# Optimization experiments

Hardware: AMD Instinct MI355X
Metric: run time of the kernel (lower is better)

Reference implementation:

```python
import jax, jax.numpy as jnp
import numpy as np
from jax import lax

T = 256        # sentence length
V = 50000      # vocab
NT = 50        # POS tags
NL = 40        # dependency labels
WD, TD = 300, 100
IN = WD + TD   # 400, LSTM input & hidden size
H = IN
BI = 2 * H     # 800, biLSTM output per token
MI = 2 * BI    # 1600, MLP input/hidden size


def setup_inputs() -> dict:
    key = jax.random.key(0)
    ks = jax.random.split(key, 32)
    s = 0.05
    d = {
        'words': jax.random.randint(ks[0], (T,), 0, V),
        'tags': jax.random.randint(ks[1], (T,), 0, NT),
        'arcs': jax.random.randint(ks[2], (T + 1,), 0, T + 1),
        'h0': jax.random.normal(ks[3], (4, 1, H), jnp.float32),
        'c0': jax.random.normal(ks[4], (4, 1, H), jnp.float32),
        'word_emb': jax.random.normal(ks[5], (V, WD), jnp.float32) * s,
        'tag_emb': jax.random.normal(ks[6], (NT, TD), jnp.float32) * s,
        # LSTM layer 0: input IN; layer 1: input BI. Leading dim 2 = directions (fwd, rev).
        'Wih0': jax.random.normal(ks[7], (2, 4 * H, IN), jnp.float32) * s,
        'Whh0': jax.random.normal(ks[8], (2, 4 * H, H), jnp.float32) * s,
        'bih0': jax.random.normal(ks[9], (2, 4 * H), jnp.float32) * s,
        'bhh0': jax.random.normal(ks[10], (2, 4 * H), jnp.float32) * s,
        'Wih1': jax.random.normal(ks[11], (2, 4 * H, BI), jnp.float32) * s,
        'Whh1': jax.random.normal(ks[12], (2, 4 * H, H), jnp.float32) * s,
        'bih1': jax.random.normal(ks[13], (2, 4 * H), jnp.float32) * s,
        'bhh1': jax.random.normal(ks[14], (2, 4 * H), jnp.float32) * s,
        # arc-score MLP: 1600 -> 1600 -> 1 (Linear, Tanh, Linear)
        'Wa1': jax.random.normal(ks[15], (MI, MI), jnp.float32) * s,
        'ba1': jax.random.normal(ks[16], (MI,), jnp.float32) * s,
        'Wa2': jax.random.normal(ks[17], (1, MI), jnp.float32) * s,
        'ba2': jax.random.normal(ks[18], (1,), jnp.float32) * s,
        # label MLP: 1600 -> 1600 -> 40
        'Wl1': jax.random.normal(ks[19], (MI, MI), jnp.float32) * s,
        'bl1': jax.random.normal(ks[20], (MI,), jnp.float32) * s,
        'Wl2': jax.random.normal(ks[21], (NL, MI), jnp.float32) * s,
        'bl2': jax.random.normal(ks[22], (NL,), jnp.float32) * s,
    }
    return d


def _lstm_dir(x, Wih, Whh, bih, bhh, h, c):
    # x: [T, in]; returns [T, H]. Torch gate order i, f, g, o.
    xg = x @ Wih.T + (bih + bhh)  # precompute input projection: [T, 4H]

    def step(carry, xt):
        h, c = carry
        g = xt + h @ Whh.T
        i, f, gg, o = jnp.split(g, 4, axis=-1)
        i, f, o = jax.nn.sigmoid(i), jax.nn.sigmoid(f), jax.nn.sigmoid(o)
        c = f * c + i * jnp.tanh(gg)
        h = o * jnp.tanh(c)
        return (h, c), h

    (_, _), ys = lax.scan(step, (h, c), xg)
    return ys


def _bilstm_layer(x, Wih, Whh, bih, bhh, h0f, c0f, h0b, c0b):
    fwd = _lstm_dir(x, Wih[0], Whh[0], bih[0], bhh[0], h0f, c0f)
    bwd = _lstm_dir(x[::-1], Wih[1], Whh[1], bih[1], bhh[1], h0b, c0b)[::-1]
    return jnp.concatenate([fwd, bwd], axis=-1)


def _mlp(z, W1, b1, W2, b2):
    return jnp.tanh(z @ W1.T + b1) @ W2.T + b2


def reference(words, tags, arcs, h0, c0, word_emb, tag_emb,
              Wih0, Whh0, bih0, bhh0, Wih1, Whh1, bih1, bhh1,
              Wa1, ba1, Wa2, ba2, Wl1, bl1, Wl2, bl2):
    n = words.shape[0]
    x = jnp.concatenate([word_emb[words], tag_emb[tags]], axis=-1)  # [T, 400]
    x1 = _bilstm_layer(x, Wih0, Whh0, bih0, bhh0, h0[0, 0], c0[0, 0], h0[1, 0], c0[1, 0])
    hV = _bilstm_layer(x1, Wih1, Whh1, bih1, bhh1, h0[2, 0], c0[2, 0], h0[3, 0], c0[3, 0])  # [T, 800]

    # All-pairs arc scores: feats[h, d] = concat(hV[h], hV[d]) -> MLP -> scalar.
    hh = jnp.broadcast_to(hV[:, None, :], (n, n, BI))
    dd = jnp.broadcast_to(hV[None, :, :], (n, n, BI))
    feats = jnp.concatenate([hh, dd], axis=-1)  # [T, T, 1600]
    raw = _mlp(feats, Wa1, ba1, Wa2, ba2)[..., 0]  # [T, T]
    raw = raw * (1.0 - jnp.eye(n, dtype=raw.dtype))  # head == dep left at 0
    scores = jnp.zeros((n + 1, n + 1), raw.dtype).at[1:, 1:].set(raw).at[0, 0].set(1.0)

    # Labels: for token i with gold head h (1-based), concat(hV[i], hV[h-1]); head==0 -> zeros.
    heads = arcs[1:]
    idx = jnp.clip(heads - 1, 0, n - 1)
    lf = jnp.concatenate([hV, hV[idx]], axis=-1)  # [T, 1600]
    lab = _mlp(lf, Wl1, bl1, Wl2, bl2)  # [T, 40]
    lab = jnp.where((heads == 0)[:, None], jnp.zeros_like(lab), lab)
    return (scores, lab)
```

## Files before the change

### kernel.cpp

```cpp
#include <hip/hip_runtime.h>

typedef unsigned int   u32;
typedef unsigned long long u64;

__device__ __forceinline__ float fast_tanh(float x) {
    x = fminf(fmaxf(x, -15.f), 15.f);
    float e = __expf(2.f * x);
    return __fdividef(e - 1.f, e + 1.f);
}

#define OF_XG   ((size_t)0)
#define OF_H    (OF_XG + 3276800)
#define OF_PQ   (OF_H  + 1638400)
#define OF_U    (OF_PQ + 3276800)

__device__ __forceinline__ float4 hist4(const u64* __restrict__ hist, int t, int k) {
    const u64* p = (k < 400) ? hist + (size_t)t * 400 + k
                             : hist + 102400 + (size_t)(255 - t) * 400 + (k - 400);
    ulonglong2 a = *(const ulonglong2*)p;
    ulonglong2 b = *(const ulonglong2*)(p + 2);
    return make_float4(__uint_as_float((u32)a.x), __uint_as_float((u32)a.y),
                       __uint_as_float((u32)b.x), __uint_as_float((u32)b.y));
}

__global__ __launch_bounds__(256)
void gemm_embed_kernel(const int* __restrict__ words, const int* __restrict__ tags,
                       const float* __restrict__ wemb, const float* __restrict__ temb,
                       const float* __restrict__ B,
                       const float* __restrict__ bias1, const float* __restrict__ bias2,
                       float* __restrict__ C) {
    int t0 = blockIdx.x * 64;
    int n0 = blockIdx.y * 64;
    int tid = threadIdx.x;
    int tx = tid & 15, ty = tid >> 4;
    int lr = tid >> 2, lk = (tid & 3) * 4;
    __shared__ float As[16][68];
    __shared__ float Bs[16][68];
    float acc[4][4] = {};

    int t = t0 + lr;
    const float* arow0 = wemb + (size_t)words[t] * 300;
    const float* arow1 = temb + (size_t)tags[t] * 100 - 300;

    for (int k0 = 0; k0 < 400; k0 += 16) {
        int k = k0 + lk;
        float4 av = (k < 300) ? *(const float4*)(arow0 + k) : *(const float4*)(arow1 + k);
        float4 bv = *(const float4*)(B + (size_t)(n0 + lr) * 400 + k);
        __syncthreads();
        As[lk + 0][lr] = av.x; As[lk + 1][lr] = av.y; As[lk + 2][lr] = av.z; As[lk + 3][lr] = av.w;
        Bs[lk + 0][lr] = bv.x; Bs[lk + 1][lr] = bv.y; Bs[lk + 2][lr] = bv.z; Bs[lk + 3][lr] = bv.w;
        __syncthreads();
        #pragma unroll
        for (int kk = 0; kk < 16; ++kk) {
            float4 a4 = *(const float4*)&As[kk][ty * 4];
            float4 b4 = *(const float4*)&Bs[kk][tx * 4];
            acc[0][0] += a4.x * b4.x; acc[0][1] += a4.x * b4.y; acc[0][2] += a4.x * b4.z; acc[0][3] += a4.x * b4.w;
            acc[1][0] += a4.y * b4.x; acc[1][1] += a4.y * b4.y; acc[1][2] += a4.y * b4.z; acc[1][3] += a4.y * b4.w;
            acc[2][0] += a4.z * b4.x; acc[2][1] += a4.z * b4.y; acc[2][2] += a4.z * b4.z; acc[2][3] += a4.z * b4.w;
            acc[3][0] += a4.w * b4.x; acc[3][1] += a4.w * b4.y; acc[3][2] += a4.w * b4.z; acc[3][3] += a4.w * b4.w;
        }
    }
    float bs[4];
    #pragma unroll
    for (int j = 0; j < 4; ++j) {
        int n = n0 + tx * 4 + j;
        bs[j] = bias1[n] + bias2[n];
    }
    #pragma unroll
    for (int i = 0; i < 4; ++i) {
        int tr = t0 + ty * 4 + i;
        float4 o;
        o.x = acc[i][0] + bs[0]; o.y = acc[i][1] + bs[1];
        o.z = acc[i][2] + bs[2]; o.w = acc[i][3] + bs[3];
        *(float4*)(C + (size_t)tr * 3200 + n0 + tx * 4) = o;
    }
}

__global__ __launch_bounds__(256)
void gemm_hist_kernel(const u64* __restrict__ hist, const int* __restrict__ arcs,
                      const float* __restrict__ B, int ldb, int boff,
                      const float* __restrict__ bias1, const float* __restrict__ bias2,
                      float* __restrict__ C, int ldc, int K, int act) {
    int t0 = blockIdx.x * 64;
    int n0 = blockIdx.y * 64;
    int tid = threadIdx.x;
    int tx = tid & 15, ty = tid >> 4;
    int lr = tid >> 2, lk = (tid & 3) * 4;
    __shared__ float As[16][68];
    __shared__ float Bs[16][68];
    float acc[4][4] = {};

    int t = t0 + lr;
    int tind = t;
    if (arcs) {
        int h = arcs[1 + t];
        tind = min(max(h - 1, 0), 255);
    }

    for (int k0 = 0; k0 < K; k0 += 16) {
        int k = k0 + lk;
        int tt = (k < 800) ? t : tind;
        int kk2 = (k < 800) ? k : k - 800;
        float4 av = hist4(hist, tt, kk2);
        float4 bv = *(const float4*)(B + (size_t)(n0 + lr) * ldb + boff + k0 + lk);
        __syncthreads();
        As[lk + 0][lr] = av.x; As[lk + 1][lr] = av.y; As[lk + 2][lr] = av.z; As[lk + 3][lr] = av.w;
        Bs[lk + 0][lr] = bv.x; Bs[lk + 1][lr] = bv.y; Bs[lk + 2][lr] = bv.z; Bs[lk + 3][lr] = bv.w;
        __syncthreads();
        #pragma unroll
        for (int kk = 0; kk < 16; ++kk) {
            float4 a4 = *(const float4*)&As[kk][ty * 4];
            float4 b4 = *(const float4*)&Bs[kk][tx * 4];
            acc[0][0] += a4.x * b4.x; acc[0][1] += a4.x * b4.y; acc[0][2] += a4.x * b4.z; acc[0][3] += a4.x * b4.w;
            acc[1][0] += a4.y * b4.x; acc[1][1] += a4.y * b4.y; acc[1][2] += a4.y * b4.z; acc[1][3] += a4.y * b4.w;
            acc[2][0] += a4.z * b4.x; acc[2][1] += a4.z * b4.y; acc[2][2] += a4.z * b4.z; acc[2][3] += a4.z * b4.w;
            acc[3][0] += a4.w * b4.x; acc[3][1] += a4.w * b4.y; acc[3][2] += a4.w * b4.z; acc[3][3] += a4.w * b4.w;
        }
    }
    float bs[4];
    #pragma unroll
    for (int j = 0; j < 4; ++j) {
        int n = n0 + tx * 4 + j;
        float b = 0.f;
        if (bias1) b += bias1[n];
        if (bias2) b += bias2[n];
        bs[j] = b;
    }
    #pragma unroll
    for (int i = 0; i < 4; ++i) {
        int tr = t0 + ty * 4 + i;
        float4 o;
        o.x = acc[i][0] + bs[0]; o.y = acc[i][1] + bs[1];
        o.z = acc[i][2] + bs[2]; o.w = acc[i][3] + bs[3];
        if (act) { o.x = fast_tanh(o.x); o.y = fast_tanh(o.y); o.z = fast_tanh(o.z); o.w = fast_tanh(o.w); }
        *(float4*)(C + (size_t)tr * ldc + n0 + tx * 4) = o;
    }
}

__global__ __launch_bounds__(256)
void gemm_pq_kernel(const u64* __restrict__ hist, const float* __restrict__ Wa1,
                    const float* __restrict__ ba1, float* __restrict__ PQ) {
    int t0 = blockIdx.x * 64;
    int n0 = blockIdx.y * 64;
    int tid = threadIdx.x;
    int tx = tid & 15, ty = tid >> 4;
    int lr = tid >> 2, lk = (tid & 3) * 4;
    __shared__ float As[16][68];
    __shared__ float Bs[16][68];
    float acc[4][4] = {};

    int t = t0 + lr;
    int nn = n0 + lr;
    const float* brow = (nn < 1600) ? Wa1 + (size_t)nn * 1600
                                    : Wa1 + (size_t)(nn - 1600) * 1600 + 800;

    for (int k0 = 0; k0 < 800; k0 += 16) {
        float4 av = hist4(hist, t, k0 + lk);
        float4 bv = *(const float4*)(brow + k0 + lk);
        __syncthreads();
        As[lk + 0][lr] = av.x; As[lk + 1][lr] = av.y; As[lk + 2][lr] = av.z; As[lk + 3][lr] = av.w;
        Bs[lk + 0][lr] = bv.x; Bs[lk + 1][lr] = bv.y; Bs[lk + 2][lr] = bv.z; Bs[lk + 3][lr] = bv.w;
        __syncthreads();
        #pragma unroll
        for (int kk = 0; kk < 16; ++kk) {
            float4 a4 = *(const float4*)&As[kk][ty * 4];
            float4 b4 = *(const float4*)&Bs[kk][tx * 4];
            acc[0][0] += a4.x * b4.x; acc[0][1] += a4.x * b4.y; acc[0][2] += a4.x * b4.z; acc[0][3] += a4.x * b4.w;
            acc[1][0] += a4.y * b4.x; acc[1][1] += a4.y * b4.y; acc[1][2] += a4.y * b4.z; acc[1][3] += a4.y * b4.w;
            acc[2][0] += a4.z * b4.x; acc[2][1] += a4.z * b4.y; acc[2][2] += a4.z * b4.z; acc[2][3] += a4.z * b4.w;
            acc[3][0] += a4.w * b4.x; acc[3][1] += a4.w * b4.y; acc[3][2] += a4.w * b4.z; acc[3][3] += a4.w * b4.w;
        }
    }
    float bs[4];
    #pragma unroll
    for (int j = 0; j < 4; ++j) {
        int n = n0 + tx * 4 + j;
        bs[j] = (n < 1600) ? ba1[n] : 0.f;
    }
    #pragma unroll
    for (int i = 0; i < 4; ++i) {
        int tr = t0 + ty * 4 + i;
        float4 o;
        o.x = acc[i][0] + bs[0]; o.y = acc[i][1] + bs[1];
        o.z = acc[i][2] + bs[2]; o.w = acc[i][3] + bs[3];
        *(float4*)(PQ + (size_t)tr * 3200 + n0 + tx * 4) = o;
    }
}

#define LSTM_G 50
__global__ __launch_bounds__(256)
void lstm_kernel(const float* __restrict__ Whh,
                 const float* __restrict__ h0,
                 const float* __restrict__ c0,
                 int hc_base,
                 const float* __restrict__ xg,
                 u64* __restrict__ hist,
                 u32 tag_base) {
    const int T = 256;
    int bid = blockIdx.x;
    int d  = bid / LSTM_G;
    int wg = bid % LSTM_G;
    int a8 = wg * 8;
    int tid = threadIdx.x;
    int w = tid >> 6, lane = tid & 63;
    int c = lane & 7, r = lane >> 3;
    int gate = r >> 1, jj = r & 1;
    int gr = gate * 400 + a8 + 2 * w + jj;

    __shared__ float hbuf[2][416];

    float4 wv[13];
    const float* wrow = Whh + (size_t)d * 640000 + (size_t)gr * 400;
    #pragma unroll
    for (int i = 0; i < 13; ++i) {
        int k = 4 * (c + 8 * i);
        wv[i] = (k + 3 < 400) ? *(const float4*)(wrow + k) : make_float4(0.f, 0.f, 0.f, 0.f);
    }
    if (tid < 16) { hbuf[0][400 + tid] = 0.f; hbuf[1][400 + tid] = 0.f; }

    float c_state = 0.f;
    if (lane == 0 || lane == 8)
        c_state = c0[(hc_base + d) * 400 + a8 + 2 * w + jj];

    u64* hst = hist + (size_t)d * 102400;
    bool need2 = (tid + 256 < 400);

    for (int t = 0; t < T; ++t) {
        int xt = d ? (T - 1 - t) : t;
        float xgv = xg[(size_t)xt * 3200 + d * 1600 + gr];
        float* hb = hbuf[t & 1];

        if (t == 0) {
            hb[tid] = h0[(hc_base + d) * 400 + tid];
            if (need2) hb[tid + 256] = h0[(hc_base + d) * 400 + tid + 256];
        } else {
            const u64* src = hst + (size_t)(t - 1) * 400;
            u32 want = tag_base + (u32)t;
            bool d1 = false, d2 = !need2;
            while (!(d1 && d2)) {
                u64 v1 = 0, v2 = 0;
                if (!d1) v1 = __hip_atomic_load(&src[tid], __ATOMIC_RELAXED, __HIP_MEMORY_SCOPE_AGENT);
                if (!d2) v2 = __hip_atomic_load(&src[tid + 256], __ATOMIC_RELAXED, __HIP_MEMORY_SCOPE_AGENT);
                if (!d1 && (u32)(v1 >> 32) == want) { hb[tid] = __uint_as_float((u32)v1); d1 = true; }
                if (!d2 && (u32)(v2 >> 32) == want) { hb[tid + 256] = __uint_as_float((u32)v2); d2 = true; }
            }
        }
        __syncthreads();

        const float4* h4 = (const float4*)hb;
        float s = 0.f;
        #pragma unroll
        for (int i = 0; i < 13; ++i) {
            float4 hv = h4[c + 8 * i];
            s += wv[i].x * hv.x + wv[i].y * hv.y + wv[i].z * hv.z + wv[i].w * hv.w;
        }
        s += __shfl_down(s, 4);
        s += __shfl_down(s, 2);
        s += __shfl_down(s, 1);

        float v = 0.f;
        if (c == 0) {
            float tot = s + xgv;
            float arg = (gate == 2) ? 2.f * tot : -tot;
            arg = fminf(fmaxf(arg, -60.f), 60.f);
            float e = __expf(arg);
            v = (gate == 2) ? (e - 1.f) * __frcp_rn(e + 1.f)
                            : __frcp_rn(1.f + e);
        }
        float fv = __shfl(v, lane + 16);
        float gv = __shfl(v, lane + 32);
        float ov = __shfl(v, lane + 48);
        if (lane == 0 || lane == 8) {
            c_state = fv * c_state + v * gv;
            float ec = __expf(fminf(fmaxf(2.f * c_state, -60.f), 60.f));
            float th = (ec - 1.f) * __frcp_rn(ec + 1.f);
            float h = ov * th;
            u64 pk = (((u64)(tag_base + t + 1)) << 32) | (u64)__float_as_uint(h);
            __hip_atomic_store(&hst[(size_t)t * 400 + a8 + 2 * w + jj], pk,
                               __ATOMIC_RELAXED, __HIP_MEMORY_SCOPE_AGENT);
        }
    }
}

__global__ __launch_bounds__(256)
void arc_kernel(const float* __restrict__ PQ,
                const float* __restrict__ Wa2, const float* __restrict__ ba2,
                float* __restrict__ out) {
    int i0 = blockIdx.x * 16, j0 = blockIdx.y * 16;
    int tid = threadIdx.x;
    int ii = tid >> 4, jj = tid & 15;
    __shared__ float Pt[16][65], Qt[16][65];
    __shared__ float W2f[1600];

    if (i0 == 0 && j0 == 0) {
        if (tid < 257) out[tid] = (tid == 0) ? 1.0f : 0.0f;
        out[(size_t)(tid + 1) * 257] = 0.0f;
        if (tid == 0) out[0] = 1.0f;
    }
    for (int m = tid; m < 1600; m += 256) W2f[m] = Wa2[m];
    __syncthreads();

    float acc = 0.f;
    int mm = tid & 63, r4 = tid >> 6;
    for (int m0 = 0; m0 < 1600; m0 += 64) {
        #pragma unroll
        for (int rr = r4; rr < 16; rr += 4) {
            Pt[rr][mm] = PQ[(size_t)(i0 + rr) * 3200 + m0 + mm];
            Qt[rr][mm] = PQ[(size_t)(j0 + rr) * 3200 + 1600 + m0 + mm];
        }
        __syncthreads();
        #pragma unroll 8
        for (int m = 0; m < 64; ++m) {
            float s = Pt[ii][m] + Qt[jj][m];
            acc += W2f[m0 + m] * fast_tanh(s);
        }
        __syncthreads();
    }
    float raw = acc + ba2[0];
    int gi = i0 + ii, gj = j0 + jj;
    if (gi == gj) raw = 0.f;
    out[(size_t)(gi + 1) * 257 + (gj + 1)] = raw;
}

__global__ __launch_bounds__(256)
void label_out_kernel(const float* __restrict__ U, const float* __restrict__ Wl2,
                      const float* __restrict__ bl2, const int* __restrict__ arcs,
                      float* __restrict__ out) {
    int t = blockIdx.x;
    __shared__ float u_l[1600];
    __shared__ float part[4][64];
    for (int m = threadIdx.x; m < 1600; m += 256) u_l[m] = U[(size_t)t * 1600 + m];
    __syncthreads();
    int tid = threadIdx.x;
    int n = tid & 63, p = tid >> 6;
    float acc = 0.f;
    if (n < 40) {
        const float4* wr4 = (const float4*)(Wl2 + (size_t)n * 1600 + p * 400);
        const float*  ub  = u_l + p * 400;
        for (int m = 0; m < 100; ++m) {
            float4 w = wr4[m];
            acc += ub[4*m] * w.x + ub[4*m+1] * w.y + ub[4*m+2] * w.z + ub[4*m+3] * w.w;
        }
    }
    part[p][n] = acc;
    __syncthreads();
    if (tid < 40) {
        float v = part[0][tid] + part[1][tid] + part[2][tid] + part[3][tid] + bl2[tid];
        if (arcs[1 + t] == 0) v = 0.f;
        out[(size_t)t * 40 + tid] = v;
    }
}

extern "C" void kernel_launch(void* const* d_in, const int* in_sizes, int n_in,
                              void* d_out, int out_size, void* d_ws, size_t ws_size,
                              hipStream_t stream) {
    const int*   words = (const int*)d_in[0];
    const int*   tags  = (const int*)d_in[1];
    const int*   arcs  = (const int*)d_in[2];
    const float* h0    = (const float*)d_in[3];
    const float* c0    = (const float*)d_in[4];
    const float* wemb  = (const float*)d_in[5];
    const float* temb  = (const float*)d_in[6];
    const float* Wih0  = (const float*)d_in[7];
    const float* Whh0  = (const float*)d_in[8];
    const float* bih0  = (const float*)d_in[9];
    const float* bhh0  = (const float*)d_in[10];
    const float* Wih1  = (const float*)d_in[11];
    const float* Whh1  = (const float*)d_in[12];
    const float* bih1  = (const float*)d_in[13];
    const float* bhh1  = (const float*)d_in[14];
    const float* Wa1   = (const float*)d_in[15];
    const float* ba1   = (const float*)d_in[16];
    const float* Wa2   = (const float*)d_in[17];
    const float* ba2   = (const float*)d_in[18];
    const float* Wl1   = (const float*)d_in[19];
    const float* bl1   = (const float*)d_in[20];
    const float* Wl2   = (const float*)d_in[21];
    const float* bl2   = (const float*)d_in[22];
    float* out = (float*)d_out;

    char* ws = (char*)d_ws;
    float* xg   = (float*)(ws + OF_XG);
    u64*   hist = (u64*)  (ws + OF_H);
    float* PQ   = (float*)(ws + OF_PQ);
    float* U    = (float*)(ws + OF_U);

    gemm_embed_kernel<<<dim3(4, 50), 256, 0, stream>>>(words, tags, wemb, temb, Wih0, bih0, bhh0, xg);
    lstm_kernel<<<2 * LSTM_G, 256, 0, stream>>>(Whh0, h0, c0, 0, xg, hist, 0u);
    gemm_hist_kernel<<<dim3(4, 50), 256, 0, stream>>>(hist, nullptr, Wih1, 800, 0, bih1, bhh1, xg, 3200, 800, 0);
    lstm_kernel<<<2 * LSTM_G, 256, 0, stream>>>(Whh1, h0, c0, 2, xg, hist, 256u);
    gemm_pq_kernel<<<dim3(4, 50), 256, 0, stream>>>(hist, Wa1, ba1, PQ);
    arc_kernel<<<dim3(16, 16), 256, 0, stream>>>(PQ, Wa2, ba2, out);
    gemm_hist_kernel<<<dim3(4, 25), 256, 0, stream>>>(hist, arcs, Wl1, 1600, 0, bl1, nullptr, U, 1600, 1600, 1);
    label_out_kernel<<<256, 256, 0, stream>>>(U, Wl2, bl2, arcs, out + 66049);
}
```

Baseline: 1.268 ms.

## Halve LSTM workgroups, two hidden units per lane, vectorized 16-byte polling

The recurrent LSTM kernel now runs 25 workgroups per direction instead of 50. Each lane holds two weight rows and computes two hidden units, which halves the number of cross-workgroup participants in each per-step handoff. Polling for the previous step's hidden state uses an inline-asm 16-byte cache-bypassing load that checks two tagged values at once, so 200 threads poll instead of up to 400. The cost is twice the weight registers per thread and fewer workgroups running in parallel.

```diff
diff --git a/kernel.cpp b/kernel.cpp
--- a/kernel.cpp
+++ b/kernel.cpp
@@ -2,11 +2,19 @@
 
 typedef unsigned int   u32;
 typedef unsigned long long u64;
+typedef unsigned int u32x4 __attribute__((ext_vector_type(4)));
 
 __device__ __forceinline__ float fast_tanh(float x) {
     x = fminf(fmaxf(x, -15.f), 15.f);
     float e = __expf(2.f * x);
     return __fdividef(e - 1.f, e + 1.f);
+}
+
+__device__ __forceinline__ u32x4 poll16(const u64* p) {
+    u32x4 r;
+    asm volatile("global_load_dwordx4 %0, %1, off sc0 sc1\n\ts_waitcnt vmcnt(0)"
+                 : "=v"(r) : "v"(p) : "memory");
+    return r;
 }
 
 #define OF_XG   ((size_t)0)
@@ -187,7 +195,7 @@
     }
 }
 
-#define LSTM_G 50
+#define LSTM_G 25
 __global__ __launch_bounds__(256)
 void lstm_kernel(const float* __restrict__ Whh,
                  const float* __restrict__ h0,
@@ -200,83 +208,112 @@
     int bid = blockIdx.x;
     int d  = bid / LSTM_G;
     int wg = bid % LSTM_G;
-    int a8 = wg * 8;
+    int a16 = wg * 16;
     int tid = threadIdx.x;
     int w = tid >> 6, lane = tid & 63;
     int c = lane & 7, r = lane >> 3;
-    int gate = r >> 1, jj = r & 1;
-    int gr = gate * 400 + a8 + 2 * w + jj;
+    int gate = r >> 1, half = r & 1;
+    int ub  = a16 + 4 * w + half * 2;
+    int grA = gate * 400 + ub;
 
     __shared__ float hbuf[2][416];
 
-    float4 wv[13];
-    const float* wrow = Whh + (size_t)d * 640000 + (size_t)gr * 400;
+    float4 wvA[13], wvB[13];
+    const float* rowA = Whh + (size_t)d * 640000 + (size_t)grA * 400;
+    const float* rowB = rowA + 400;
     #pragma unroll
     for (int i = 0; i < 13; ++i) {
         int k = 4 * (c + 8 * i);
-        wv[i] = (k + 3 < 400) ? *(const float4*)(wrow + k) : make_float4(0.f, 0.f, 0.f, 0.f);
+        if (k + 3 < 400) { wvA[i] = *(const float4*)(rowA + k); wvB[i] = *(const float4*)(rowB + k); }
+        else             { wvA[i] = make_float4(0.f,0.f,0.f,0.f); wvB[i] = make_float4(0.f,0.f,0.f,0.f); }
     }
     if (tid < 16) { hbuf[0][400 + tid] = 0.f; hbuf[1][400 + tid] = 0.f; }
 
-    float c_state = 0.f;
-    if (lane == 0 || lane == 8)
-        c_state = c0[(hc_base + d) * 400 + a8 + 2 * w + jj];
+    float cA = 0.f, cB = 0.f;
+    if (c == 0 && gate == 0) {
+        cA = c0[(hc_base + d) * 400 + ub];
+        cB = c0[(hc_base + d) * 400 + ub + 1];
+    }
 
     u64* hst = hist + (size_t)d * 102400;
-    bool need2 = (tid + 256 < 400);
 
     for (int t = 0; t < T; ++t) {
         int xt = d ? (T - 1 - t) : t;
-        float xgv = xg[(size_t)xt * 3200 + d * 1600 + gr];
+        float2 xg2 = *(const float2*)(xg + (size_t)xt * 3200 + d * 1600 + grA);
         float* hb = hbuf[t & 1];
 
         if (t == 0) {
             hb[tid] = h0[(hc_base + d) * 400 + tid];
-            if (need2) hb[tid + 256] = h0[(hc_base + d) * 400 + tid + 256];
-        } else {
-            const u64* src = hst + (size_t)(t - 1) * 400;
+            if (tid < 144) hb[tid + 256] = h0[(hc_base + d) * 400 + tid + 256];
+        } else if (tid < 200) {
+            const u64* src = hst + (size_t)(t - 1) * 400 + 2 * tid;
             u32 want = tag_base + (u32)t;
-            bool d1 = false, d2 = !need2;
-            while (!(d1 && d2)) {
-                u64 v1 = 0, v2 = 0;
-                if (!d1) v1 = __hip_atomic_load(&src[tid], __ATOMIC_RELAXED, __HIP_MEMORY_SCOPE_AGENT);
-                if (!d2) v2 = __hip_atomic_load(&src[tid + 256], __ATOMIC_RELAXED, __HIP_MEMORY_SCOPE_AGENT);
-                if (!d1 && (u32)(v1 >> 32) == want) { hb[tid] = __uint_as_float((u32)v1); d1 = true; }
-                if (!d2 && (u32)(v2 >> 32) == want) { hb[tid + 256] = __uint_as_float((u32)v2); d2 = true; }
+            for (;;) {
+                u32x4 v = poll16(src);
+                if (v.y == want && v.w == want) {
+                    hb[2 * tid]     = __uint_as_float(v.x);
+                    hb[2 * tid + 1] = __uint_as_float(v.z);
+                    break;
+                }
             }
         }
         __syncthreads();
 
         const float4* h4 = (const float4*)hb;
-        float s = 0.f;
+        float a0 = 0.f, a1 = 0.f, b0 = 0.f, b1 = 0.f;
         #pragma unroll
         for (int i = 0; i < 13; ++i) {
             float4 hv = h4[c + 8 * i];
-            s += wv[i].x * hv.x + wv[i].y * hv.y + wv[i].z * hv.z + wv[i].w * hv.w;
-        }
-        s += __shfl_down(s, 4);
-        s += __shfl_down(s, 2);
-        s += __shfl_down(s, 1);
-
-        float v = 0.f;
+            float4 wa = wvA[i], wb = wvB[i];
+            if (i & 1) {
+                a1 += wa.x * hv.x + wa.y * hv.y + wa.z * hv.z + wa.w * hv.w;
+                b1 += wb.x * hv.x + wb.y * hv.y + wb.z * hv.z + wb.w * hv.w;
+            } else {
+                a0 += wa.x * hv.x + wa.y * hv.y + wa.z * hv.z + wa.w * hv.w;
+                b0 += wb.x * hv.x + wb.y * hv.y + wb.z * hv.z + wb.w * hv.w;
+            }
+        }
+        float sA = a0 + a1, sB = b0 + b1;
+        sA += __shfl_down(sA, 4); sB += __shfl_down(sB, 4);
+        sA += __shfl_down(sA, 2); sB += __shfl_down(sB, 2);
+        sA += __shfl_down(sA, 1); sB += __shfl_down(sB, 1);
+
+        float vA = 0.f, vB = 0.f;
         if (c == 0) {
-            float tot = s + xgv;
-            float arg = (gate == 2) ? 2.f * tot : -tot;
-            arg = fminf(fmaxf(arg, -60.f), 60.f);
-            float e = __expf(arg);
-            v = (gate == 2) ? (e - 1.f) * __frcp_rn(e + 1.f)
-                            : __frcp_rn(1.f + e);
-        }
-        float fv = __shfl(v, lane + 16);
-        float gv = __shfl(v, lane + 32);
-        float ov = __shfl(v, lane + 48);
-        if (lane == 0 || lane == 8) {
-            c_state = fv * c_state + v * gv;
-            float ec = __expf(fminf(fmaxf(2.f * c_state, -60.f), 60.f));
-            float th = (ec - 1.f) * __frcp_rn(ec + 1.f);
-            float h = ov * th;
-            u64 pk = (((u64)(tag_base + t + 1)) << 32) | (u64)__float_as_uint(h);
-            __hip_atomic_store(&hst[(size_t)t * 400 + a8 + 2 * w + jj], pk,
+            float totA = sA + xg2.x;
+            float totB = sB + xg2.y;
+            float argA = (gate == 2) ? 2.f * totA : -totA;
+            float argB = (gate == 2) ? 2.f * totB : -totB;
+            argA = fminf(fmaxf(argA, -60.f), 60.f);
+            argB = fminf(fmaxf(argB, -60.f), 60.f);
+            float eA = __expf(argA), eB = __expf(argB);
+            if (gate == 2) {
+                vA = (eA - 1.f) * __frcp_rn(eA + 1.f);
+                vB = (eB - 1.f) * __frcp_rn(eB + 1.f);
+            } else {
+                vA = __frcp_rn(1.f + eA);
+                vB = __frcp_rn(1.f + eB);
+            }
+        }
+        float fA = __shfl(vA, lane + 16);
+        float gA = __shfl(vA, lane + 32);
+        float oA = __shfl(vA, lane + 48);
+        float fB = __shfl(vB, lane + 16);
+        float gB = __shfl(vB, lane + 32);
+        float oB = __shfl(vB, lane + 48);
+        if (c == 0 && gate == 0) {
+            cA = fA * cA + vA * gA;
+            cB = fB * cB + vB * gB;
+            float ecA = __expf(fminf(fmaxf(2.f * cA, -60.f), 60.f));
+            float ecB = __expf(fminf(fmaxf(2.f * cB, -60.f), 60.f));
+            float hA = oA * ((ecA - 1.f) * __frcp_rn(ecA + 1.f));
+            float hB = oB * ((ecB - 1.f) * __frcp_rn(ecB + 1.f));
+            u64 tagw = ((u64)(tag_base + t + 1)) << 32;
+            u64 pkA = tagw | (u64)__float_as_uint(hA);
+            u64 pkB = tagw | (u64)__float_as_uint(hB);
+            __hip_atomic_store(&hst[(size_t)t * 400 + ub],     pkA,
+                               __ATOMIC_RELAXED, __HIP_MEMORY_SCOPE_AGENT);
+            __hip_atomic_store(&hst[(size_t)t * 400 + ub + 1], pkB,
                                __ATOMIC_RELAXED, __HIP_MEMORY_SCOPE_AGENT);
         }
     }
```

Measured after the change: 1.703 ms. +34.3%, slower.
